# Kernel optimization log

Hardware: AMD Instinct MI355X
Metric: run time of the kernel (lower is better)

The kernel has to match this reference:

```python
import jax, jax.numpy as jnp
import numpy as np

N_HEADS = 8; N_LEVELS = 4; T_WINDOW = 2; N_CURR = 4; N_TEMP = 2; D_MODEL = 256
D_HEAD = D_MODEL // N_HEADS
SHAPES = [[4, 32, 48], [4, 16, 24], [4, 8, 12], [4, 4, 6]]  # (T, H, W) per level
LEN_IN = sum(t * h * w for t, h, w in SHAPES)  # 8160
LEN_Q = LEN_IN
N_BATCH = 1


def _bilinear_sample(value_l, loc):
    # value_l: (N, M, H, W, D); loc: (N, M, Q, P, 2) normalized to [0, 1].
    # Matches torch grid_sample(mode='bilinear', padding_mode='zeros', align_corners=False)
    # with grid = 2*loc - 1, i.e. pixel coords x = loc_x*W - 0.5, y = loc_y*H - 0.5.
    N, M, H, W, D = value_l.shape
    Q, P = loc.shape[2], loc.shape[3]
    x = loc[..., 0] * W - 0.5
    y = loc[..., 1] * H - 0.5
    x0 = jnp.floor(x); y0 = jnp.floor(y)
    wx = x - x0; wy = y - y0
    flat = value_l.reshape(N, M, H * W, D)

    def gather(xi, yi):
        valid = ((xi >= 0) & (xi < W) & (yi >= 0) & (yi < H)).astype(value_l.dtype)
        idx = (jnp.clip(yi, 0, H - 1) * W + jnp.clip(xi, 0, W - 1)).astype(jnp.int32)
        g = jnp.take_along_axis(flat, idx.reshape(N, M, Q * P, 1), axis=2)
        return g.reshape(N, M, Q, P, D) * valid[..., None]

    v00 = gather(x0, y0); v10 = gather(x0 + 1.0, y0)
    v01 = gather(x0, y0 + 1.0); v11 = gather(x0 + 1.0, y0 + 1.0)
    return (v00 * ((1 - wx) * (1 - wy))[..., None] + v10 * (wx * (1 - wy))[..., None]
            + v01 * ((1 - wx) * wy)[..., None] + v11 * (wx * wy)[..., None])


def _forward(query, reference_points, temporal_offsets, input_flatten, shapes, starts,
             Wv, bv, Ws, bs, Wa, ba, Wts, bts, Wta, bta, Wo, bo):
    N, Lq, _ = query.shape
    value = (input_flatten @ Wv + bv).reshape(N, -1, N_HEADS, D_HEAD)
    ts_off = (query @ Wts + bts).reshape(N, Lq, N_HEADS, N_LEVELS, T_WINDOW, N_TEMP, 2)
    t_attn = (query @ Wta + bta).reshape(N, Lq, N_HEADS, N_LEVELS * T_WINDOW * N_TEMP)
    c_attn = (query @ Wa + ba).reshape(N, Lq, N_HEADS, N_LEVELS * N_CURR)
    # joint softmax over current + temporal sampling points (as in the source)
    attn = jax.nn.softmax(jnp.concatenate([c_attn, t_attn], axis=-1), axis=-1)
    aw_c = attn[..., :N_LEVELS * N_CURR].reshape(N, Lq, N_HEADS, N_LEVELS, N_CURR)
    aw_t = attn[..., N_LEVELS * N_CURR:].reshape(N, Lq, N_HEADS, N_LEVELS, T_WINDOW * N_TEMP)
    aw = jnp.concatenate([aw_c, aw_t], axis=4)  # (N, Lq, M, L, P)
    c_off = (query @ Ws + bs).reshape(N, Lq, N_HEADS, N_LEVELS, N_CURR, 2)
    # flattened-temporal grid per level: width W_l, height T_l*H_l
    norm = jnp.array([[w, t * h] for t, h, w in shapes], dtype=query.dtype)  # (L, 2)
    loc_c = reference_points[:, :, None, :, None, :] + c_off / norm[None, None, None, :, None, :]
    loc_t = (reference_points[:, :, None, :, None, None, :]
             + temporal_offsets[:, :, None, :, :, None, :]
             + ts_off / norm[None, None, None, :, None, None, :])
    loc_t = loc_t.reshape(N, Lq, N_HEADS, N_LEVELS, T_WINDOW * N_TEMP, 2)
    locs = jnp.concatenate([loc_c, loc_t], axis=4)  # (N, Lq, M, L, P, 2)
    out = jnp.zeros((N, N_HEADS, Lq, D_HEAD), query.dtype)
    for l, (t, h, w) in enumerate(shapes):
        s = starts[l]
        vl = value[:, s:s + t * h * w].transpose(0, 2, 1, 3).reshape(N, N_HEADS, t * h, w, D_HEAD)
        loc_l = locs[:, :, :, l].transpose(0, 2, 1, 3, 4)   # (N, M, Lq, P, 2)
        sampled = _bilinear_sample(vl, loc_l)               # (N, M, Lq, P, Dh)
        w_l = aw[:, :, :, l].transpose(0, 2, 1, 3)          # (N, M, Lq, P)
        out = out + jnp.einsum('nmqpd,nmqp->nmqd', sampled, w_l)
    out = out.transpose(0, 2, 1, 3).reshape(N, Lq, D_MODEL)
    return out @ Wo + bo


def setup_inputs() -> dict:
    key = jax.random.key(0)
    ks = jax.random.split(key, 18)
    D = D_MODEL
    sc = 0.02
    query = jax.random.normal(ks[0], (N_BATCH, LEN_Q, D), jnp.float32)
    reference_points = jax.random.uniform(ks[1], (N_BATCH, LEN_Q, N_LEVELS, 2), jnp.float32)
    temporal_offsets = jax.random.uniform(ks[2], (N_BATCH, LEN_Q, N_LEVELS, T_WINDOW, 2),
                                          jnp.float32, minval=-0.25, maxval=0.25)
    input_flatten = jax.random.normal(ks[3], (N_BATCH, LEN_IN, D), jnp.float32)
    input_spatial_shapes = jnp.array(SHAPES, dtype=jnp.int32)
    starts = np.cumsum([0] + [t * h * w for t, h, w in SHAPES])[:-1]
    input_level_start_index = jnp.array(starts, dtype=jnp.int32)
    n_off = N_HEADS * N_LEVELS * N_CURR * 2          # 256
    n_att = N_HEADS * N_LEVELS * N_CURR              # 128
    n_toff = N_HEADS * N_LEVELS * T_WINDOW * N_TEMP * 2  # 256
    n_tatt = N_HEADS * N_LEVELS * T_WINDOW * N_TEMP      # 128
    return {
        'query': query, 'reference_points': reference_points,
        'temporal_offsets': temporal_offsets, 'input_flatten': input_flatten,
        'input_spatial_shapes': input_spatial_shapes,
        'input_level_start_index': input_level_start_index,
        'Wv': jax.random.normal(ks[4], (D, D), jnp.float32) * sc,
        'bv': jnp.zeros((D,), jnp.float32),
        'Ws': jax.random.normal(ks[5], (D, n_off), jnp.float32) * sc,
        'bs': jax.random.normal(ks[6], (n_off,), jnp.float32) * 2.0,
        'Wa': jax.random.normal(ks[7], (D, n_att), jnp.float32) * sc,
        'ba': jnp.zeros((n_att,), jnp.float32),
        'Wts': jax.random.normal(ks[8], (D, n_toff), jnp.float32) * sc,
        'bts': jax.random.normal(ks[9], (n_toff,), jnp.float32) * 2.0,
        'Wta': jax.random.normal(ks[10], (D, n_tatt), jnp.float32) * sc,
        'bta': jnp.zeros((n_tatt,), jnp.float32),
        'Wo': jax.random.normal(ks[11], (D, D), jnp.float32) * sc,
        'bo': jnp.zeros((D,), jnp.float32),
    }


def reference(query, reference_points, temporal_offsets, input_flatten,
              input_spatial_shapes, input_level_start_index,
              Wv, bv, Ws, bs, Wa, ba, Wts, bts, Wta, bta, Wo, bo):
    shapes = [tuple(int(v) for v in row) for row in np.asarray(input_spatial_shapes)]
    starts = [int(v) for v in np.asarray(input_level_start_index)]
    return _forward(query, reference_points, temporal_offsets, input_flatten,
                    shapes, starts, Wv, bv, Ws, bs, Wa, ba, Wts, bts, Wta, bta, Wo, bo)
```

## Files before the change

### kernel.cpp

```cpp
#include <hip/hip_runtime.h>


#define LEN 8160

typedef __attribute__((ext_vector_type(8))) short bf16x8;
typedef __attribute__((ext_vector_type(4))) float f32x4;

__device__ __forceinline__ void split_bf16(float v, unsigned short* hi, unsigned short* lo)
{
    unsigned u = __float_as_uint(v);
    unsigned r = (u + 0x7FFFu + ((u >> 16) & 1u)) & 0xFFFF0000u;
    float hif = __uint_as_float(r);
    float lof = v - hif;
    unsigned ul = __float_as_uint(lof);
    unsigned rl = (ul + 0x7FFFu + ((ul >> 16) & 1u)) >> 16;
    *hi = (unsigned short)(r >> 16);
    *lo = (unsigned short)rl;
}

__global__ __launch_bounds__(256) void pack_kernel(
    const float* __restrict__ Ws, const float* __restrict__ bs,
    const float* __restrict__ Wa, const float* __restrict__ ba,
    const float* __restrict__ Wts, const float* __restrict__ bts,
    const float* __restrict__ Wta, const float* __restrict__ bta,
    const float* __restrict__ Wv, const float* __restrict__ Wo,
    unsigned short* __restrict__ Whi, unsigned short* __restrict__ Wlo,
    float* __restrict__ bcat)
{
    int idx = blockIdx.x * 256 + threadIdx.x;
    if (idx < 1280 * 256) {
        int n = idx >> 8, k = idx & 255;
        float v;
        if (n < 256) v = Wv[k * 256 + n];
        else if (n < 1024) {
            int j = n - 256;
            if (j < 256)      v = Ws [k * 256 + j];
            else if (j < 384) v = Wa [k * 128 + (j - 256)];
            else if (j < 640) v = Wts[k * 256 + (j - 384)];
            else              v = Wta[k * 128 + (j - 640)];
        } else v = Wo[k * 256 + (n - 1024)];
        unsigned short h, l; split_bf16(v, &h, &l);
        Whi[idx] = h; Wlo[idx] = l;
    } else if (idx < 1280 * 256 + 768) {
        int j = idx - 1280 * 256;
        float v;
        if (j < 256)      v = bs[j];
        else if (j < 384) v = ba[j - 256];
        else if (j < 640) v = bts[j - 384];
        else              v = bta[j - 640];
        bcat[j] = v;
    }
}

__global__ __launch_bounds__(256) void convA_kernel(
    const float* __restrict__ inpf, const float* __restrict__ query,
    unsigned short* __restrict__ Ahi, unsigned short* __restrict__ Alo,
    unsigned short* __restrict__ Qhi, unsigned short* __restrict__ Qlo)
{
    int idx = blockIdx.x * 256 + threadIdx.x;
    int which = (idx >= LEN * 256) ? 1 : 0;
    int off = idx - which * (LEN * 256);
    float v = which ? query[off] : inpf[off];
    unsigned short h, l; split_bf16(v, &h, &l);
    if (which) { Qhi[off] = h; Qlo[off] = l; }
    else       { Ahi[off] = h; Alo[off] = l; }
}

__global__ __launch_bounds__(256) void gemm_mfma_kernel(
    const unsigned short* __restrict__ Ahi, const unsigned short* __restrict__ Alo,
    const unsigned short* __restrict__ Bhi, const unsigned short* __restrict__ Blo,
    const float* __restrict__ bias, float* __restrict__ C, int M, int N)
{
    __shared__ unsigned short BsH[64][72];
    __shared__ unsigned short BsL[64][72];
    const int tid = threadIdx.x;
    const int wave = tid >> 6, lane = tid & 63;
    const int bx = blockIdx.x, by = blockIdx.y;
    const int lm = lane & 15;
    const int kq = lane >> 4;

    const int m = by * 64 + wave * 16 + lm;
    const unsigned short* aHp = Ahi + (size_t)m * 256 + kq * 8;
    const unsigned short* aLp = Alo + (size_t)m * 256 + kq * 8;

    const int sn = tid >> 2;
    const int sk = (tid & 3) * 16;
    const unsigned short* bHs = Bhi + (size_t)(bx * 64 + sn) * 256 + sk;
    const unsigned short* bLs = Blo + (size_t)(bx * 64 + sn) * 256 + sk;

    f32x4 acc[4] = {};
    for (int kc = 0; kc < 4; kc++) {
        *(uint4*)(&BsH[sn][sk])     = *(const uint4*)(bHs + kc * 64);
        *(uint4*)(&BsH[sn][sk + 8]) = *(const uint4*)(bHs + kc * 64 + 8);
        *(uint4*)(&BsL[sn][sk])     = *(const uint4*)(bLs + kc * 64);
        *(uint4*)(&BsL[sn][sk + 8]) = *(const uint4*)(bLs + kc * 64 + 8);
        __syncthreads();
        #pragma unroll
        for (int kt = 0; kt < 2; kt++) {
            const int ko = kc * 64 + kt * 32;
            bf16x8 ah = *(const bf16x8*)(aHp + ko);
            bf16x8 al = *(const bf16x8*)(aLp + ko);
            #pragma unroll
            for (int nt = 0; nt < 4; nt++) {
                bf16x8 bh = *(const bf16x8*)(&BsH[nt * 16 + lm][kt * 32 + kq * 8]);
                bf16x8 bl = *(const bf16x8*)(&BsL[nt * 16 + lm][kt * 32 + kq * 8]);
                acc[nt] = __builtin_amdgcn_mfma_f32_16x16x32_bf16(ah, bh, acc[nt], 0, 0, 0);
                acc[nt] = __builtin_amdgcn_mfma_f32_16x16x32_bf16(ah, bl, acc[nt], 0, 0, 0);
                acc[nt] = __builtin_amdgcn_mfma_f32_16x16x32_bf16(al, bh, acc[nt], 0, 0, 0);
            }
        }
        __syncthreads();
    }
    const int row0 = by * 64 + wave * 16 + kq * 4;
    const int col = bx * 64 + lm;
    #pragma unroll
    for (int nt = 0; nt < 4; nt++) {
        float bb = bias[col + nt * 16];
        #pragma unroll
        for (int r = 0; r < 4; r++) {
            int row = row0 + r;
            if (row < M)
                C[(size_t)row * N + col + nt * 16] = acc[nt][r] + bb;
        }
    }
}

__global__ __launch_bounds__(256) void sample_kernel(
    const float* __restrict__ value,
    const float* __restrict__ proj,
    const float* __restrict__ refp,
    const float* __restrict__ toff,
    unsigned short* __restrict__ attn_hi,
    unsigned short* __restrict__ attn_lo)
{
    const int q = blockIdx.x;
    const int head = threadIdx.x >> 5;
    const int lane = threadIdx.x & 31;
    __shared__ int4   s_idx[8][32];
    __shared__ float4 s_w[8][32];

    const float* p = proj + (size_t)q * 768;

    {
        const int i = lane;
        float logit, ox, oy, rx, ry;
        int l;
        if (i < 16) {
            l = i >> 2; int pt2 = i & 3;
            logit = p[256 + head * 16 + i];
            ox = p[head * 32 + l * 8 + pt2 * 2 + 0];
            oy = p[head * 32 + l * 8 + pt2 * 2 + 1];
            rx = refp[q * 8 + l * 2 + 0];
            ry = refp[q * 8 + l * 2 + 1];
        } else {
            int j = i - 16; l = j >> 2;
            int tp = j & 3, tw = tp >> 1, nt = tp & 1;
            logit = p[640 + head * 16 + j];
            ox = p[384 + head * 32 + l * 8 + tw * 4 + nt * 2 + 0];
            oy = p[384 + head * 32 + l * 8 + tw * 4 + nt * 2 + 1];
            rx = refp[q * 8 + l * 2 + 0] + toff[q * 16 + l * 4 + tw * 2 + 0];
            ry = refp[q * 8 + l * 2 + 1] + toff[q * 16 + l * 4 + tw * 2 + 1];
        }
        const int Wl = 48 >> l;
        const int Hgl = 128 >> l;
        const int st = 8192 - (8192 >> (2 * l));
        const float fW = (float)Wl, fHg = (float)Hgl;
        float x = (rx + ox / fW) * fW - 0.5f;
        float y = (ry + oy / fHg) * fHg - 0.5f;

        float mx = logit;
        #pragma unroll
        for (int off = 16; off > 0; off >>= 1)
            mx = fmaxf(mx, __shfl_xor(mx, off, 32));
        float e = expf(logit - mx);
        float s = e;
        #pragma unroll
        for (int off = 16; off > 0; off >>= 1)
            s += __shfl_xor(s, off, 32);
        float w = e / s;

        float fx = floorf(x), fy = floorf(y);
        float wx = x - fx, wy = y - fy;
        int x0 = (int)fx, y0 = (int)fy;
        int x1 = x0 + 1, y1 = y0 + 1;
        float m00 = ((unsigned)x0 < (unsigned)Wl && (unsigned)y0 < (unsigned)Hgl) ? 1.f : 0.f;
        float m10 = ((unsigned)x1 < (unsigned)Wl && (unsigned)y0 < (unsigned)Hgl) ? 1.f : 0.f;
        float m01 = ((unsigned)x0 < (unsigned)Wl && (unsigned)y1 < (unsigned)Hgl) ? 1.f : 0.f;
        float m11 = ((unsigned)x1 < (unsigned)Wl && (unsigned)y1 < (unsigned)Hgl) ? 1.f : 0.f;
        int cx0 = min(max(x0, 0), Wl - 1), cx1 = min(max(x1, 0), Wl - 1);
        int cy0 = min(max(y0, 0), Hgl - 1), cy1 = min(max(y1, 0), Hgl - 1);
        int4 ii;
        ii.x = (st + cy0 * Wl + cx0) * 256;
        ii.y = (st + cy0 * Wl + cx1) * 256;
        ii.z = (st + cy1 * Wl + cx0) * 256;
        ii.w = (st + cy1 * Wl + cx1) * 256;
        float sx0 = 1.f - wx, sy0 = 1.f - wy;
        float4 ww;
        ww.x = w * sx0 * sy0 * m00;
        ww.y = w * wx  * sy0 * m10;
        ww.z = w * sx0 * wy  * m01;
        ww.w = w * wx  * wy  * m11;
        s_idx[head][lane] = ii;
        s_w[head][lane] = ww;
    }
    __syncthreads();

    const float* vh = value + head * 32 + lane;
    float acc = 0.f;
    #pragma unroll 4
    for (int i = 0; i < 32; i++) {
        int4 ii = s_idx[head][i];
        float4 ww = s_w[head][i];
        acc = fmaf(ww.x, vh[ii.x], acc);
        acc = fmaf(ww.y, vh[ii.y], acc);
        acc = fmaf(ww.z, vh[ii.z], acc);
        acc = fmaf(ww.w, vh[ii.w], acc);
    }
    unsigned short h, l; split_bf16(acc, &h, &l);
    size_t o = (size_t)q * 256 + head * 32 + lane;
    attn_hi[o] = h;
    attn_lo[o] = l;
}

extern "C" void kernel_launch(void* const* d_in, const int* in_sizes, int n_in,
                              void* d_out, int out_size, void* d_ws, size_t ws_size,
                              hipStream_t stream)
{
    const float* query = (const float*)d_in[0];
    const float* refp  = (const float*)d_in[1];
    const float* toff  = (const float*)d_in[2];
    const float* inpf  = (const float*)d_in[3];
    const float* Wv  = (const float*)d_in[6];
    const float* bv  = (const float*)d_in[7];
    const float* Ws_ = (const float*)d_in[8];
    const float* bs_ = (const float*)d_in[9];
    const float* Wa  = (const float*)d_in[10];
    const float* ba  = (const float*)d_in[11];
    const float* Wts = (const float*)d_in[12];
    const float* bts = (const float*)d_in[13];
    const float* Wta = (const float*)d_in[14];
    const float* bta = (const float*)d_in[15];
    const float* Wo  = (const float*)d_in[16];
    const float* bo  = (const float*)d_in[17];
    float* out = (float*)d_out;

    float* ws    = (float*)d_ws;
    float* value = ws;
    float* proj  = value + (size_t)LEN * 256;
    float* bcat  = proj + (size_t)LEN * 768;
    unsigned short* Whi = (unsigned short*)(bcat + 768);
    unsigned short* Wlo = Whi + 1280 * 256;
    unsigned short* Ahi = Wlo + 1280 * 256;
    unsigned short* Alo = Ahi + 8192 * 256;
    unsigned short* Qhi = Alo + 8192 * 256;
    unsigned short* Qlo = Qhi + 8192 * 256;

    dim3 blk(256);
    pack_kernel<<<1284, blk, 0, stream>>>(Ws_, bs_, Wa, ba, Wts, bts, Wta, bta,
                                          Wv, Wo, Whi, Wlo, bcat);
    convA_kernel<<<2 * LEN, blk, 0, stream>>>(inpf, query, Ahi, Alo, Qhi, Qlo);
    gemm_mfma_kernel<<<dim3(4, 128), blk, 0, stream>>>(Ahi, Alo, Whi, Wlo,
                                                       bv, value, LEN, 256);
    gemm_mfma_kernel<<<dim3(12, 128), blk, 0, stream>>>(Qhi, Qlo,
                                                        Whi + 256 * 256, Wlo + 256 * 256,
                                                        bcat, proj, LEN, 768);
    sample_kernel<<<LEN, blk, 0, stream>>>(value, proj, refp, toff, Ahi, Alo);
    gemm_mfma_kernel<<<dim3(4, 128), blk, 0, stream>>>(Ahi, Alo,
                                                       Whi + 1024 * 256, Wlo + 1024 * 256,
                                                       bo, out, LEN, 256);
}
```

Before: 196.5 us.

## Merge prep kernels, fuse value and projection GEMMs, vectorize sampling gathers

Three changes. The weight-pack and activation-convert kernels become one launch. The value GEMM and the query projection GEMM are merged into a single grid that picks its operands by blockIdx.x. The sampling kernel now gathers float4 per lane, splitting 32 points over four lane groups, then reduces across lanes with shuffles and writes packed bf16 pairs. The aim is to cut launch count and tail effects and to issue wider, fewer memory gathers in sampling, at the cost of extra shuffles and idle lanes during the final store.

Result: faster. 188.0 us (-4.3%).

```diff
diff --git a/kernel.cpp b/kernel.cpp
--- a/kernel.cpp
+++ b/kernel.cpp
@@ -2,6 +2,8 @@
 
 
 #define LEN 8160
+#define NCONV (2 * LEN * 256)
+#define NPACK (1280 * 256)
 
 typedef __attribute__((ext_vector_type(8))) short bf16x8;
 typedef __attribute__((ext_vector_type(4))) float f32x4;
@@ -18,18 +20,29 @@
     *lo = (unsigned short)rl;
 }
 
-__global__ __launch_bounds__(256) void pack_kernel(
+__global__ __launch_bounds__(256) void prep_kernel(
+    const float* __restrict__ inpf, const float* __restrict__ query,
     const float* __restrict__ Ws, const float* __restrict__ bs,
     const float* __restrict__ Wa, const float* __restrict__ ba,
     const float* __restrict__ Wts, const float* __restrict__ bts,
     const float* __restrict__ Wta, const float* __restrict__ bta,
     const float* __restrict__ Wv, const float* __restrict__ Wo,
+    unsigned short* __restrict__ Ahi, unsigned short* __restrict__ Alo,
+    unsigned short* __restrict__ Qhi, unsigned short* __restrict__ Qlo,
     unsigned short* __restrict__ Whi, unsigned short* __restrict__ Wlo,
     float* __restrict__ bcat)
 {
     int idx = blockIdx.x * 256 + threadIdx.x;
-    if (idx < 1280 * 256) {
-        int n = idx >> 8, k = idx & 255;
+    if (idx < NCONV) {
+        int which = (idx >= LEN * 256) ? 1 : 0;
+        int off = idx - which * (LEN * 256);
+        float v = which ? query[off] : inpf[off];
+        unsigned short h, l; split_bf16(v, &h, &l);
+        if (which) { Qhi[off] = h; Qlo[off] = l; }
+        else       { Ahi[off] = h; Alo[off] = l; }
+    } else if (idx < NCONV + NPACK) {
+        int j2 = idx - NCONV;
+        int n = j2 >> 8, k = j2 & 255;
         float v;
         if (n < 256) v = Wv[k * 256 + n];
         else if (n < 1024) {
@@ -40,9 +53,9 @@
             else              v = Wta[k * 128 + (j - 640)];
         } else v = Wo[k * 256 + (n - 1024)];
         unsigned short h, l; split_bf16(v, &h, &l);
-        Whi[idx] = h; Wlo[idx] = l;
-    } else if (idx < 1280 * 256 + 768) {
-        int j = idx - 1280 * 256;
+        Whi[j2] = h; Wlo[j2] = l;
+    } else if (idx < NCONV + NPACK + 768) {
+        int j = idx - (NCONV + NPACK);
         float v;
         if (j < 256)      v = bs[j];
         else if (j < 384) v = ba[j - 256];
@@ -52,30 +65,32 @@
     }
 }
 
-__global__ __launch_bounds__(256) void convA_kernel(
-    const float* __restrict__ inpf, const float* __restrict__ query,
-    unsigned short* __restrict__ Ahi, unsigned short* __restrict__ Alo,
-    unsigned short* __restrict__ Qhi, unsigned short* __restrict__ Qlo)
-{
-    int idx = blockIdx.x * 256 + threadIdx.x;
-    int which = (idx >= LEN * 256) ? 1 : 0;
-    int off = idx - which * (LEN * 256);
-    float v = which ? query[off] : inpf[off];
-    unsigned short h, l; split_bf16(v, &h, &l);
-    if (which) { Qhi[off] = h; Qlo[off] = l; }
-    else       { Ahi[off] = h; Alo[off] = l; }
-}
-
-__global__ __launch_bounds__(256) void gemm_mfma_kernel(
-    const unsigned short* __restrict__ Ahi, const unsigned short* __restrict__ Alo,
-    const unsigned short* __restrict__ Bhi, const unsigned short* __restrict__ Blo,
-    const float* __restrict__ bias, float* __restrict__ C, int M, int N)
+__global__ __launch_bounds__(256) void gemm_mfma_dual(
+    const unsigned short* __restrict__ A0hi, const unsigned short* __restrict__ A0lo,
+    const unsigned short* __restrict__ B0hi, const unsigned short* __restrict__ B0lo,
+    const float* __restrict__ bias0, float* __restrict__ C0, int N0, int nbx0,
+    const unsigned short* __restrict__ A1hi, const unsigned short* __restrict__ A1lo,
+    const unsigned short* __restrict__ B1hi, const unsigned short* __restrict__ B1lo,
+    const float* __restrict__ bias1, float* __restrict__ C1, int N1)
 {
     __shared__ unsigned short BsH[64][72];
     __shared__ unsigned short BsL[64][72];
     const int tid = threadIdx.x;
     const int wave = tid >> 6, lane = tid & 63;
-    const int bx = blockIdx.x, by = blockIdx.y;
+    int bx = blockIdx.x;
+    const int by = blockIdx.y;
+
+    const unsigned short *Ahi, *Alo, *Bhi, *Blo;
+    const float* bias; float* C; int N;
+    if (bx < nbx0) {
+        Ahi = A0hi; Alo = A0lo; Bhi = B0hi; Blo = B0lo;
+        bias = bias0; C = C0; N = N0;
+    } else {
+        bx -= nbx0;
+        Ahi = A1hi; Alo = A1lo; Bhi = B1hi; Blo = B1lo;
+        bias = bias1; C = C1; N = N1;
+    }
+
     const int lm = lane & 15;
     const int kq = lane >> 4;
 
@@ -119,7 +134,7 @@
         #pragma unroll
         for (int r = 0; r < 4; r++) {
             int row = row0 + r;
-            if (row < M)
+            if (row < LEN)
                 C[(size_t)row * N + col + nt * 16] = acc[nt][r] + bb;
         }
     }
@@ -190,10 +205,10 @@
         int cx0 = min(max(x0, 0), Wl - 1), cx1 = min(max(x1, 0), Wl - 1);
         int cy0 = min(max(y0, 0), Hgl - 1), cy1 = min(max(y1, 0), Hgl - 1);
         int4 ii;
-        ii.x = (st + cy0 * Wl + cx0) * 256;
-        ii.y = (st + cy0 * Wl + cx1) * 256;
-        ii.z = (st + cy1 * Wl + cx0) * 256;
-        ii.w = (st + cy1 * Wl + cx1) * 256;
+        ii.x = (st + cy0 * Wl + cx0) * 64;
+        ii.y = (st + cy0 * Wl + cx1) * 64;
+        ii.z = (st + cy1 * Wl + cx0) * 64;
+        ii.w = (st + cy1 * Wl + cx1) * 64;
         float sx0 = 1.f - wx, sy0 = 1.f - wy;
         float4 ww;
         ww.x = w * sx0 * sy0 * m00;
@@ -205,21 +220,45 @@
     }
     __syncthreads();
 
-    const float* vh = value + head * 32 + lane;
-    float acc = 0.f;
+    const int pt4 = lane >> 3;
+    const int c4  = lane & 7;
+    const float4* vb = (const float4*)value + head * 8 + c4;
+    float4 acc = make_float4(0.f, 0.f, 0.f, 0.f);
     #pragma unroll 4
-    for (int i = 0; i < 32; i++) {
-        int4 ii = s_idx[head][i];
-        float4 ww = s_w[head][i];
-        acc = fmaf(ww.x, vh[ii.x], acc);
-        acc = fmaf(ww.y, vh[ii.y], acc);
-        acc = fmaf(ww.z, vh[ii.z], acc);
-        acc = fmaf(ww.w, vh[ii.w], acc);
-    }
-    unsigned short h, l; split_bf16(acc, &h, &l);
-    size_t o = (size_t)q * 256 + head * 32 + lane;
-    attn_hi[o] = h;
-    attn_lo[o] = l;
+    for (int i = 0; i < 8; i++) {
+        int pidx = (i << 2) | pt4;
+        int4 ii = s_idx[head][pidx];
+        float4 ww = s_w[head][pidx];
+        float4 v0 = vb[ii.x], v1 = vb[ii.y], v2 = vb[ii.z], v3 = vb[ii.w];
+        acc.x = fmaf(ww.x, v0.x, acc.x); acc.y = fmaf(ww.x, v0.y, acc.y);
+        acc.z = fmaf(ww.x, v0.z, acc.z); acc.w = fmaf(ww.x, v0.w, acc.w);
+        acc.x = fmaf(ww.y, v1.x, acc.x); acc.y = fmaf(ww.y, v1.y, acc.y);
+        acc.z = fmaf(ww.y, v1.z, acc.z); acc.w = fmaf(ww.y, v1.w, acc.w);
+        acc.x = fmaf(ww.z, v2.x, acc.x); acc.y = fmaf(ww.z, v2.y, acc.y);
+        acc.z = fmaf(ww.z, v2.z, acc.z); acc.w = fmaf(ww.z, v2.w, acc.w);
+        acc.x = fmaf(ww.w, v3.x, acc.x); acc.y = fmaf(ww.w, v3.y, acc.y);
+        acc.z = fmaf(ww.w, v3.z, acc.z); acc.w = fmaf(ww.w, v3.w, acc.w);
+    }
+    #pragma unroll
+    for (int off = 8; off <= 16; off <<= 1) {
+        acc.x += __shfl_xor(acc.x, off, 32);
+        acc.y += __shfl_xor(acc.y, off, 32);
+        acc.z += __shfl_xor(acc.z, off, 32);
+        acc.w += __shfl_xor(acc.w, off, 32);
+    }
+    if (pt4 == 0) {
+        unsigned short h0, l0, h1, l1, h2, l2, h3, l3;
+        split_bf16(acc.x, &h0, &l0); split_bf16(acc.y, &h1, &l1);
+        split_bf16(acc.z, &h2, &l2); split_bf16(acc.w, &h3, &l3);
+        uint2 hv, lv;
+        hv.x = (unsigned)h0 | ((unsigned)h1 << 16);
+        hv.y = (unsigned)h2 | ((unsigned)h3 << 16);
+        lv.x = (unsigned)l0 | ((unsigned)l1 << 16);
+        lv.y = (unsigned)l2 | ((unsigned)l3 << 16);
+        size_t o = (size_t)q * 256 + head * 32 + c4 * 4;
+        *(uint2*)(attn_hi + o) = hv;
+        *(uint2*)(attn_lo + o) = lv;
+    }
 }
 
 extern "C" void kernel_launch(void* const* d_in, const int* in_sizes, int n_in,
@@ -256,16 +295,14 @@
     unsigned short* Qlo = Qhi + 8192 * 256;
 
     dim3 blk(256);
-    pack_kernel<<<1284, blk, 0, stream>>>(Ws_, bs_, Wa, ba, Wts, bts, Wta, bta,
-                                          Wv, Wo, Whi, Wlo, bcat);
-    convA_kernel<<<2 * LEN, blk, 0, stream>>>(inpf, query, Ahi, Alo, Qhi, Qlo);
-    gemm_mfma_kernel<<<dim3(4, 128), blk, 0, stream>>>(Ahi, Alo, Whi, Wlo,
-                                                       bv, value, LEN, 256);
-    gemm_mfma_kernel<<<dim3(12, 128), blk, 0, stream>>>(Qhi, Qlo,
-                                                        Whi + 256 * 256, Wlo + 256 * 256,
-                                                        bcat, proj, LEN, 768);
+    prep_kernel<<<17603, blk, 0, stream>>>(inpf, query, Ws_, bs_, Wa, ba,
+                                           Wts, bts, Wta, bta, Wv, Wo,
+                                           Ahi, Alo, Qhi, Qlo, Whi, Wlo, bcat);
+    gemm_mfma_dual<<<dim3(16, 128), blk, 0, stream>>>(
+        Ahi, Alo, Whi, Wlo, bv, value, 256, 4,
+        Qhi, Qlo, Whi + 256 * 256, Wlo + 256 * 256, bcat, proj, 768);
     sample_kernel<<<LEN, blk, 0, stream>>>(value, proj, refp, toff, Ahi, Alo);
-    gemm_mfma_kernel<<<dim3(4, 128), blk, 0, stream>>>(Ahi, Alo,
-                                                       Whi + 1024 * 256, Wlo + 1024 * 256,
-                                                       bo, out, LEN, 256);
-}
+    gemm_mfma_dual<<<dim3(4, 128), blk, 0, stream>>>(
+        Ahi, Alo, Whi + 1024 * 256, Wlo + 1024 * 256, bo, out, 256, 4,
+        Ahi, Alo, Whi + 1024 * 256, Wlo + 1024 * 256, bo, out, 256);
+}
```
